# Performance work log

Hardware: AMD Instinct MI355X
Metric: run time of the kernel (lower is better)

## Reference

```python
import jax, jax.numpy as jnp
import numpy as np

NUM_HEAD = 8  # matches init_kwargs num_head


def setup_inputs() -> dict:
    key = jax.random.key(0)
    ks = jax.random.split(key, 8)
    B, N, C, P = 2, 1024, 512, 256
    cluster_num = 8
    s = 0.02
    return {
        "x_token": jax.random.normal(ks[0], (B, N, C), jnp.float32),
        "x_path": jax.random.normal(ks[1], (B, N, P), jnp.float32),
        "idx_cluster": jax.random.randint(ks[2], (B, N), 0, cluster_num),
        "cluster_num": cluster_num,
        "Wq": jax.random.normal(ks[3], (C, C), jnp.float32) * s,
        "Wk": jax.random.normal(ks[4], (C, C), jnp.float32) * s,
        "Wv": jax.random.normal(ks[5], (C, C), jnp.float32) * s,
        "Wproj": jax.random.normal(ks[6], (C, C), jnp.float32) * s,
        "bproj": jnp.zeros((C,), jnp.float32),
    }


def reference(x_token, x_path, idx_cluster, cluster_num, Wq, Wk, Wv, Wproj, bproj):
    eps = 1e-6
    B, N, C = x_token.shape
    H = NUM_HEAD
    hd = C // H
    scale = hd ** -0.5

    # Linear projections (torch Linear: y = x @ W^T), qkv_bias=False
    q = x_token @ Wq.T
    k = x_token @ Wk.T
    v = (x_token @ Wv.T).reshape(B, N, H, hd).transpose(0, 2, 1, 3)  # (B,H,N,hd)

    qh = q.reshape(B, N, H, hd).transpose(0, 2, 1, 3)  # (B,H,N,hd)
    kh = k.reshape(B, N, H, hd).transpose(0, 2, 1, 3)

    # Raw scaled scores, computed once instead of per-cluster scatter/repeat
    s_ = jnp.einsum('bhid,bhjd->bhij', qh, kh) * scale  # (B,H,N,N)

    # One-hot cluster membership: (B, cluster_num, N)
    m = (idx_cluster[:, None, :] == jnp.arange(cluster_num)[None, :, None]).astype(s_.dtype)

    # attn_map[b,c,h,i,j] = s_[b,h,i,j] if idx[b,i]==c and idx[b,j]==c else 0
    attn_map = s_[:, None] * m[:, :, None, :, None] * m[:, :, None, None, :]  # (B,K,H,N,N)

    # Sum over clusters -> within-cluster scores, zeros elsewhere
    attn = attn_map.sum(axis=1)  # (B,H,N,N)

    # Custom eps-smoothed exp normalization (masked_fill on exact zeros, as in source)
    attn = jnp.where(attn == 0, jnp.float32(-1e9), attn).astype(jnp.float32)
    attn = jnp.exp(attn)
    attn = (attn + eps / N) / (attn.sum(axis=-1, keepdims=True) + eps)

    out = jnp.einsum('bhij,bhjd->bhid', attn, v)  # (B,H,N,hd)
    out = out.transpose(0, 2, 1, 3).reshape(B, N, C)
    out = out @ Wproj.T + bproj
    return out, attn_map
```

## Files before the change

### kernel.cpp

```cpp
#include <hip/hip_runtime.h>
#include <hip/hip_bf16.h>
#include <cstdint>
#include <cstddef>

#define NB   2
#define NN   1024
#define NC   512
#define NH   8
#define NHD  64
#define NK   8

typedef __attribute__((ext_vector_type(8))) short short8v;
typedef __attribute__((ext_vector_type(4))) short short4v;
typedef __attribute__((ext_vector_type(4))) float f32x4;

__device__ __forceinline__ short f2bf(float f) {
    union { float f; unsigned u; } v; v.f = f;
    unsigned r = v.u + 0x7FFFu + ((v.u >> 16) & 1u);
    return (short)(r >> 16);
}
__device__ __forceinline__ float bf2f(short s) {
    union { unsigned u; float f; } v;
    v.u = ((unsigned)(unsigned short)s) << 16;
    return v.f;
}

__global__ __launch_bounds__(256) void cast_kernel(
    const float* __restrict__ x, const float* __restrict__ wq,
    const float* __restrict__ wk, const float* __restrict__ wv,
    const float* __restrict__ wp,
    short* __restrict__ xb, short* __restrict__ wqb, short* __restrict__ wkb,
    short* __restrict__ wvb, short* __restrict__ wpb) {
    int i = blockIdx.x * 256 + threadIdx.x;
    if (i < NB * NN * NC) xb[i] = f2bf(x[i]);
    if (i < NC * NC) {
        wqb[i] = f2bf(wq[i]);
        wkb[i] = f2bf(wk[i]);
        wvb[i] = f2bf(wv[i]);
        wpb[i] = f2bf(wp[i]);
    }
}

__global__ __launch_bounds__(256) void qkv_kernel(
    const short* __restrict__ xb, const short* __restrict__ wqb,
    const short* __restrict__ wkb, const short* __restrict__ wvb,
    short* __restrict__ qb, short* __restrict__ kb, short* __restrict__ vT) {
    __shared__ short As[64][40];
    __shared__ short Bs[64][40];
    const int tid = threadIdx.x;
    const int z = blockIdx.z;
    const short* Bsrc = (z == 0) ? wqb : ((z == 1) ? wkb : wvb);
    const int m0 = blockIdx.y * 64, n0 = blockIdx.x * 64;
    const int lane = tid & 63, wave = tid >> 6;
    const int wm = wave >> 1, wn = wave & 1, quad = lane >> 4, lr = lane & 15;
    const int row = tid >> 2, c0 = (tid & 3) * 8;
    f32x4 acc[2][2] = {};
    for (int kt = 0; kt < 512; kt += 32) {
        *(short8v*)&As[row][c0] = *(const short8v*)(xb + (m0 + row) * 512 + kt + c0);
        *(short8v*)&Bs[row][c0] = *(const short8v*)(Bsrc + (n0 + row) * 512 + kt + c0);
        __syncthreads();
        short8v a0 = *(short8v*)&As[wm * 32 + lr][quad * 8];
        short8v a1 = *(short8v*)&As[wm * 32 + 16 + lr][quad * 8];
        short8v b0 = *(short8v*)&Bs[wn * 32 + lr][quad * 8];
        short8v b1 = *(short8v*)&Bs[wn * 32 + 16 + lr][quad * 8];
        acc[0][0] = __builtin_amdgcn_mfma_f32_16x16x32_bf16(a0, b0, acc[0][0], 0, 0, 0);
        acc[0][1] = __builtin_amdgcn_mfma_f32_16x16x32_bf16(a0, b1, acc[0][1], 0, 0, 0);
        acc[1][0] = __builtin_amdgcn_mfma_f32_16x16x32_bf16(a1, b0, acc[1][0], 0, 0, 0);
        acc[1][1] = __builtin_amdgcn_mfma_f32_16x16x32_bf16(a1, b1, acc[1][1], 0, 0, 0);
        __syncthreads();
    }
    for (int sm = 0; sm < 2; sm++)
        for (int sn = 0; sn < 2; sn++)
            for (int r = 0; r < 4; r++) {
                int m = m0 + wm * 32 + sm * 16 + quad * 4 + r;
                int n = n0 + wn * 32 + sn * 16 + lr;
                short v = f2bf(acc[sm][sn][r]);
                if (z == 0) qb[m * 512 + n] = v;
                else if (z == 1) kb[m * 512 + n] = v;
                else {
                    int bb = m >> 10, i = m & 1023, h = n >> 6, d = n & 63;
                    vT[(size_t)(((bb * 8 + h) * 64 + d) << 10) + i] = v;
                }
            }
}

__global__ __launch_bounds__(256) void colsum_kernel(
    const short* __restrict__ vT, float* __restrict__ colsum) {
    __shared__ float cp[8][33];
    const int blk = blockIdx.x;
    const int bh = blk >> 3, dg = blk & 7;
    const int t = threadIdx.x;
    const int dl = t >> 5, seg = t & 31;
    const short* p = vT + (((size_t)(bh * 64 + dg * 8 + dl)) << 10) + seg * 32;
    float s = 0.f;
    for (int k = 0; k < 32; k += 8) {
        short8v v = *(const short8v*)(p + k);
        for (int j = 0; j < 8; j++) s += bf2f(v[j]);
    }
    cp[dl][seg] = s;
    __syncthreads();
    if (t < 8) {
        float v = 0.f;
        for (int s2 = 0; s2 < 32; s2++) v += cp[t][s2];
        colsum[bh * 64 + dg * 8 + t] = v;
    }
}

__global__ __launch_bounds__(256) void attn_fused_kernel(
    const short* __restrict__ qb, const short* __restrict__ kb,
    const short* __restrict__ vT, const int* __restrict__ idx,
    const float* __restrict__ colsum, float* __restrict__ attn,
    short* __restrict__ oh) {
    __shared__ short Qs[32][72], Ks[64][72], Vs[64][72], Es[32][72];
    __shared__ float Ss[32][68];
    __shared__ int idxi[32], idxj[64];
    __shared__ float rowpart[32][17];
    __shared__ float invL[32], csL[64];
    const int tid = threadIdx.x;
    const int z = blockIdx.y, b = z >> 3, h = z & 7;
    const int i0 = blockIdx.x * 32;
    const int lane = tid & 63, wave = tid >> 6;
    const int wm = wave >> 1, wn = wave & 1, quad = lane >> 4, lr = lane & 15;
    const int r0 = tid >> 3, cc = (tid & 7) * 8;
    *(short8v*)&Qs[r0][cc] = *(const short8v*)(qb + (b * 1024 + i0 + r0) * 512 + h * 64 + cc);
    if (tid < 32) idxi[tid] = idx[b * 1024 + i0 + tid];
    else if (tid < 96) csL[tid - 32] = colsum[z * 64 + (tid - 32)];
    f32x4 acc_o[2] = {};
    float rsum[2] = {0.f, 0.f};
    const int rL = tid >> 4, cI = tid & 15, cL = cI * 4;
    const f32x4 zero4 = {0.f, 0.f, 0.f, 0.f};
    for (int jt = 0; jt < 16; jt++) {
        const int j0 = jt * 64;
        *(short8v*)&Ks[r0][cc]      = *(const short8v*)(kb + (b * 1024 + j0 + r0) * 512 + h * 64 + cc);
        *(short8v*)&Ks[r0 + 32][cc] = *(const short8v*)(kb + (b * 1024 + j0 + r0 + 32) * 512 + h * 64 + cc);
        *(short8v*)&Vs[r0][cc]      = *(const short8v*)(vT + ((size_t)z << 16) + (r0 << 10) + j0 + cc);
        *(short8v*)&Vs[r0 + 32][cc] = *(const short8v*)(vT + ((size_t)z << 16) + ((r0 + 32) << 10) + j0 + cc);
        if (tid < 64) idxj[tid] = idx[b * 1024 + j0 + tid];
        __syncthreads();
        f32x4 as[2] = {};
        for (int k0 = 0; k0 < 64; k0 += 32) {
            short8v a0 = *(short8v*)&Qs[wm * 16 + lr][k0 + quad * 8];
            short8v b0 = *(short8v*)&Ks[wn * 32 + lr][k0 + quad * 8];
            short8v b1 = *(short8v*)&Ks[wn * 32 + 16 + lr][k0 + quad * 8];
            as[0] = __builtin_amdgcn_mfma_f32_16x16x32_bf16(a0, b0, as[0], 0, 0, 0);
            as[1] = __builtin_amdgcn_mfma_f32_16x16x32_bf16(a0, b1, as[1], 0, 0, 0);
        }
        for (int sn = 0; sn < 2; sn++)
            for (int r = 0; r < 4; r++)
                Ss[wm * 16 + quad * 4 + r][wn * 32 + sn * 16 + lr] = as[sn][r] * 0.125f;
        __syncthreads();
        for (int ii = 0; ii < 2; ii++) {
            const int row = ii * 16 + rL;
            const int ci = idxi[row];
            f32x4 s4 = *(f32x4*)&Ss[row][cL];
            f32x4 m4;
            short4v e4;
            for (int kk = 0; kk < 4; kk++) {
                const bool in = (idxj[cL + kk] == ci);
                const float sv = s4[kk];
                m4[kk] = in ? sv : 0.f;
                const float ev = (in && sv != 0.f) ? __expf(sv) : 0.f;
                rsum[ii] += ev;
                e4[kk] = f2bf(ev);
            }
            float* base = attn + (((size_t)(b * 64 + h)) << 20) + (((size_t)(i0 + row)) << 10) + j0 + cL;
            for (int c = 0; c < 8; c++) {
                f32x4 w = (c == ci) ? m4 : zero4;
                __builtin_nontemporal_store(w, (f32x4*)(base + ((size_t)c << 23)));
            }
            *(short4v*)&Es[row][cL] = e4;
        }
        __syncthreads();
        for (int k0 = 0; k0 < 64; k0 += 32) {
            short8v a0 = *(short8v*)&Es[wm * 16 + lr][k0 + quad * 8];
            short8v b0 = *(short8v*)&Vs[wn * 32 + lr][k0 + quad * 8];
            short8v b1 = *(short8v*)&Vs[wn * 32 + 16 + lr][k0 + quad * 8];
            acc_o[0] = __builtin_amdgcn_mfma_f32_16x16x32_bf16(a0, b0, acc_o[0], 0, 0, 0);
            acc_o[1] = __builtin_amdgcn_mfma_f32_16x16x32_bf16(a0, b1, acc_o[1], 0, 0, 0);
        }
        __syncthreads();
    }
    for (int ii = 0; ii < 2; ii++) rowpart[ii * 16 + rL][cI] = rsum[ii];
    __syncthreads();
    if (tid < 32) {
        float v = 0.f;
        for (int s = 0; s < 16; s++) v += rowpart[tid][s];
        invL[tid] = 1.f / (v + 1e-6f);
    }
    __syncthreads();
    const float epsN = 1e-6f / 1024.f;
    for (int sn = 0; sn < 2; sn++)
        for (int r = 0; r < 4; r++) {
            int iLoc = wm * 16 + quad * 4 + r;
            int d = wn * 32 + sn * 16 + lr;
            float val = (acc_o[sn][r] + epsN * csL[d]) * invL[iLoc];
            oh[((size_t)(b * 1024 + i0 + iLoc)) * 512 + h * 64 + d] = f2bf(val);
        }
}

__global__ __launch_bounds__(256) void proj_kernel(
    const short* __restrict__ oh, const short* __restrict__ wpb,
    const float* __restrict__ bias, float* __restrict__ out) {
    __shared__ short As[64][40];
    __shared__ short Bs[64][40];
    const int tid = threadIdx.x;
    const int m0 = blockIdx.y * 64, n0 = blockIdx.x * 64;
    const int lane = tid & 63, wave = tid >> 6;
    const int wm = wave >> 1, wn = wave & 1, quad = lane >> 4, lr = lane & 15;
    const int row = tid >> 2, c0 = (tid & 3) * 8;
    f32x4 acc[2][2] = {};
    for (int kt = 0; kt < 512; kt += 32) {
        *(short8v*)&As[row][c0] = *(const short8v*)(oh + (m0 + row) * 512 + kt + c0);
        *(short8v*)&Bs[row][c0] = *(const short8v*)(wpb + (n0 + row) * 512 + kt + c0);
        __syncthreads();
        short8v a0 = *(short8v*)&As[wm * 32 + lr][quad * 8];
        short8v a1 = *(short8v*)&As[wm * 32 + 16 + lr][quad * 8];
        short8v b0 = *(short8v*)&Bs[wn * 32 + lr][quad * 8];
        short8v b1 = *(short8v*)&Bs[wn * 32 + 16 + lr][quad * 8];
        acc[0][0] = __builtin_amdgcn_mfma_f32_16x16x32_bf16(a0, b0, acc[0][0], 0, 0, 0);
        acc[0][1] = __builtin_amdgcn_mfma_f32_16x16x32_bf16(a0, b1, acc[0][1], 0, 0, 0);
        acc[1][0] = __builtin_amdgcn_mfma_f32_16x16x32_bf16(a1, b0, acc[1][0], 0, 0, 0);
        acc[1][1] = __builtin_amdgcn_mfma_f32_16x16x32_bf16(a1, b1, acc[1][1], 0, 0, 0);
        __syncthreads();
    }
    for (int sm = 0; sm < 2; sm++)
        for (int sn = 0; sn < 2; sn++)
            for (int r = 0; r < 4; r++) {
                int m = m0 + wm * 32 + sm * 16 + quad * 4 + r;
                int n = n0 + wn * 32 + sn * 16 + lr;
                out[(size_t)m * 512 + n] = acc[sm][sn][r] + bias[n];
            }
}

extern "C" void kernel_launch(void* const* d_in, const int* in_sizes, int n_in,
                              void* d_out, int out_size, void* d_ws, size_t ws_size,
                              hipStream_t stream) {
    const float* x     = (const float*)d_in[0];
    const int*   idx   = (const int*)d_in[2];
    const float* Wq    = (const float*)d_in[4];
    const float* Wk    = (const float*)d_in[5];
    const float* Wv    = (const float*)d_in[6];
    const float* Wp    = (const float*)d_in[7];
    const float* bproj = (const float*)d_in[8];

    float* out  = (float*)d_out;
    float* attn = out + (size_t)NB * NN * NC;

    char* ws = (char*)d_ws;
    short* xb  = (short*)(ws + 0);
    short* wqb = (short*)(ws + 2097152);
    short* wkb = (short*)(ws + 2621440);
    short* wvb = (short*)(ws + 3145728);
    short* wpb = (short*)(ws + 3670016);
    short* qb  = (short*)(ws + 4194304);
    short* kb  = (short*)(ws + 6291456);
    short* vT  = (short*)(ws + 8388608);
    short* oh  = (short*)(ws + 10485760);
    float* colsum = (float*)(ws + 12582912);

    cast_kernel<<<4096, 256, 0, stream>>>(x, Wq, Wk, Wv, Wp, xb, wqb, wkb, wvb, wpb);
    qkv_kernel<<<dim3(8, 32, 3), 256, 0, stream>>>(xb, wqb, wkb, wvb, qb, kb, vT);
    colsum_kernel<<<128, 256, 0, stream>>>(vT, colsum);
    attn_fused_kernel<<<dim3(32, 16), 256, 0, stream>>>(qb, kb, vT, idx, colsum, attn, oh);
    proj_kernel<<<dim3(8, 32, 1), 256, 0, stream>>>(oh, wpb, bproj, out);
}
```

Before: 615.2 us.

## Fuse casts and colsum into GEMM/attention kernels, buffer attn_map rows in LDS

```diff
diff --git a/kernel.cpp b/kernel.cpp
--- a/kernel.cpp
+++ b/kernel.cpp
@@ -24,40 +24,32 @@
     v.u = ((unsigned)(unsigned short)s) << 16;
     return v.f;
 }
-
-__global__ __launch_bounds__(256) void cast_kernel(
+__device__ __forceinline__ short8v cvt8(const float* p) {
+    float4 a = *(const float4*)p;
+    float4 b = *(const float4*)(p + 4);
+    short8v r;
+    r[0] = f2bf(a.x); r[1] = f2bf(a.y); r[2] = f2bf(a.z); r[3] = f2bf(a.w);
+    r[4] = f2bf(b.x); r[5] = f2bf(b.y); r[6] = f2bf(b.z); r[7] = f2bf(b.w);
+    return r;
+}
+
+__global__ __launch_bounds__(256) void qkv_kernel(
     const float* __restrict__ x, const float* __restrict__ wq,
     const float* __restrict__ wk, const float* __restrict__ wv,
-    const float* __restrict__ wp,
-    short* __restrict__ xb, short* __restrict__ wqb, short* __restrict__ wkb,
-    short* __restrict__ wvb, short* __restrict__ wpb) {
-    int i = blockIdx.x * 256 + threadIdx.x;
-    if (i < NB * NN * NC) xb[i] = f2bf(x[i]);
-    if (i < NC * NC) {
-        wqb[i] = f2bf(wq[i]);
-        wkb[i] = f2bf(wk[i]);
-        wvb[i] = f2bf(wv[i]);
-        wpb[i] = f2bf(wp[i]);
-    }
-}
-
-__global__ __launch_bounds__(256) void qkv_kernel(
-    const short* __restrict__ xb, const short* __restrict__ wqb,
-    const short* __restrict__ wkb, const short* __restrict__ wvb,
     short* __restrict__ qb, short* __restrict__ kb, short* __restrict__ vT) {
     __shared__ short As[64][40];
     __shared__ short Bs[64][40];
     const int tid = threadIdx.x;
     const int z = blockIdx.z;
-    const short* Bsrc = (z == 0) ? wqb : ((z == 1) ? wkb : wvb);
+    const float* Bsrc = (z == 0) ? wq : ((z == 1) ? wk : wv);
     const int m0 = blockIdx.y * 64, n0 = blockIdx.x * 64;
     const int lane = tid & 63, wave = tid >> 6;
     const int wm = wave >> 1, wn = wave & 1, quad = lane >> 4, lr = lane & 15;
     const int row = tid >> 2, c0 = (tid & 3) * 8;
     f32x4 acc[2][2] = {};
     for (int kt = 0; kt < 512; kt += 32) {
-        *(short8v*)&As[row][c0] = *(const short8v*)(xb + (m0 + row) * 512 + kt + c0);
-        *(short8v*)&Bs[row][c0] = *(const short8v*)(Bsrc + (n0 + row) * 512 + kt + c0);
+        *(short8v*)&As[row][c0] = cvt8(x + (m0 + row) * 512 + kt + c0);
+        *(short8v*)&Bs[row][c0] = cvt8(Bsrc + (n0 + row) * 512 + kt + c0);
         __syncthreads();
         short8v a0 = *(short8v*)&As[wm * 32 + lr][quad * 8];
         short8v a1 = *(short8v*)&As[wm * 32 + 16 + lr][quad * 8];
@@ -84,122 +76,115 @@
             }
 }
 
-__global__ __launch_bounds__(256) void colsum_kernel(
-    const short* __restrict__ vT, float* __restrict__ colsum) {
-    __shared__ float cp[8][33];
-    const int blk = blockIdx.x;
-    const int bh = blk >> 3, dg = blk & 7;
-    const int t = threadIdx.x;
-    const int dl = t >> 5, seg = t & 31;
-    const short* p = vT + (((size_t)(bh * 64 + dg * 8 + dl)) << 10) + seg * 32;
-    float s = 0.f;
-    for (int k = 0; k < 32; k += 8) {
-        short8v v = *(const short8v*)(p + k);
-        for (int j = 0; j < 8; j++) s += bf2f(v[j]);
-    }
-    cp[dl][seg] = s;
-    __syncthreads();
-    if (t < 8) {
-        float v = 0.f;
-        for (int s2 = 0; s2 < 32; s2++) v += cp[t][s2];
-        colsum[bh * 64 + dg * 8 + t] = v;
-    }
-}
-
 __global__ __launch_bounds__(256) void attn_fused_kernel(
     const short* __restrict__ qb, const short* __restrict__ kb,
     const short* __restrict__ vT, const int* __restrict__ idx,
-    const float* __restrict__ colsum, float* __restrict__ attn,
-    short* __restrict__ oh) {
-    __shared__ short Qs[32][72], Ks[64][72], Vs[64][72], Es[32][72];
-    __shared__ float Ss[32][68];
-    __shared__ int idxi[32], idxj[64];
-    __shared__ float rowpart[32][17];
-    __shared__ float invL[32], csL[64];
+    float* __restrict__ attn, short* __restrict__ oh) {
+    __shared__ short Sm[16][1032];
+    __shared__ short Qs[16][72], Ks[64][72], Vs[64][72], Es[16][72];
+    __shared__ float Ss[16][68];
+    __shared__ float rowpart[16][17];
+    __shared__ float cpart[64][5];
+    __shared__ float invL[16], csL[64];
+    __shared__ int idxi[16], idxj[64];
     const int tid = threadIdx.x;
     const int z = blockIdx.y, b = z >> 3, h = z & 7;
-    const int i0 = blockIdx.x * 32;
+    const int i0 = blockIdx.x * 16;
     const int lane = tid & 63, wave = tid >> 6;
-    const int wm = wave >> 1, wn = wave & 1, quad = lane >> 4, lr = lane & 15;
-    const int r0 = tid >> 3, cc = (tid & 7) * 8;
-    *(short8v*)&Qs[r0][cc] = *(const short8v*)(qb + (b * 1024 + i0 + r0) * 512 + h * 64 + cc);
-    if (tid < 32) idxi[tid] = idx[b * 1024 + i0 + tid];
-    else if (tid < 96) csL[tid - 32] = colsum[z * 64 + (tid - 32)];
-    f32x4 acc_o[2] = {};
-    float rsum[2] = {0.f, 0.f};
+    const int quad = lane >> 4, lr = lane & 15;
+    const int r0 = tid >> 3, cc8 = (tid & 7) * 8;
     const int rL = tid >> 4, cI = tid & 15, cL = cI * 4;
-    const f32x4 zero4 = {0.f, 0.f, 0.f, 0.f};
+    {
+        int rq = tid >> 4, cq = (tid & 15) * 4;
+        *(short4v*)&Qs[rq][cq] = *(const short4v*)(qb + (b * 1024 + i0 + rq) * 512 + h * 64 + cq);
+    }
+    if (tid < 16) idxi[tid] = idx[b * 1024 + i0 + tid];
+    f32x4 acc_o = {};
+    float rsum = 0.f;
+    float csum = 0.f;
     for (int jt = 0; jt < 16; jt++) {
         const int j0 = jt * 64;
-        *(short8v*)&Ks[r0][cc]      = *(const short8v*)(kb + (b * 1024 + j0 + r0) * 512 + h * 64 + cc);
-        *(short8v*)&Ks[r0 + 32][cc] = *(const short8v*)(kb + (b * 1024 + j0 + r0 + 32) * 512 + h * 64 + cc);
-        *(short8v*)&Vs[r0][cc]      = *(const short8v*)(vT + ((size_t)z << 16) + (r0 << 10) + j0 + cc);
-        *(short8v*)&Vs[r0 + 32][cc] = *(const short8v*)(vT + ((size_t)z << 16) + ((r0 + 32) << 10) + j0 + cc);
+        *(short8v*)&Ks[r0][cc8]      = *(const short8v*)(kb + (b * 1024 + j0 + r0) * 512 + h * 64 + cc8);
+        *(short8v*)&Ks[r0 + 32][cc8] = *(const short8v*)(kb + (b * 1024 + j0 + r0 + 32) * 512 + h * 64 + cc8);
+        *(short8v*)&Vs[r0][cc8]      = *(const short8v*)(vT + ((size_t)z << 16) + (r0 << 10) + j0 + cc8);
+        *(short8v*)&Vs[r0 + 32][cc8] = *(const short8v*)(vT + ((size_t)z << 16) + ((r0 + 32) << 10) + j0 + cc8);
         if (tid < 64) idxj[tid] = idx[b * 1024 + j0 + tid];
         __syncthreads();
-        f32x4 as[2] = {};
+        {
+            const int d = tid >> 2, sg = (tid & 3) * 16;
+            for (int u = 0; u < 16; u++) csum += bf2f(Vs[d][sg + u]);
+        }
+        f32x4 as = {};
         for (int k0 = 0; k0 < 64; k0 += 32) {
-            short8v a0 = *(short8v*)&Qs[wm * 16 + lr][k0 + quad * 8];
-            short8v b0 = *(short8v*)&Ks[wn * 32 + lr][k0 + quad * 8];
-            short8v b1 = *(short8v*)&Ks[wn * 32 + 16 + lr][k0 + quad * 8];
-            as[0] = __builtin_amdgcn_mfma_f32_16x16x32_bf16(a0, b0, as[0], 0, 0, 0);
-            as[1] = __builtin_amdgcn_mfma_f32_16x16x32_bf16(a0, b1, as[1], 0, 0, 0);
-        }
-        for (int sn = 0; sn < 2; sn++)
-            for (int r = 0; r < 4; r++)
-                Ss[wm * 16 + quad * 4 + r][wn * 32 + sn * 16 + lr] = as[sn][r] * 0.125f;
-        __syncthreads();
-        for (int ii = 0; ii < 2; ii++) {
-            const int row = ii * 16 + rL;
-            const int ci = idxi[row];
-            f32x4 s4 = *(f32x4*)&Ss[row][cL];
-            f32x4 m4;
-            short4v e4;
+            short8v a0 = *(short8v*)&Qs[lr][k0 + quad * 8];
+            short8v b0 = *(short8v*)&Ks[wave * 16 + lr][k0 + quad * 8];
+            as = __builtin_amdgcn_mfma_f32_16x16x32_bf16(a0, b0, as, 0, 0, 0);
+        }
+        for (int r = 0; r < 4; r++)
+            Ss[quad * 4 + r][wave * 16 + lr] = as[r] * 0.125f;
+        __syncthreads();
+        {
+            const int ci = idxi[rL];
+            f32x4 s4 = *(f32x4*)&Ss[rL][cL];
+            short4v m4b, e4;
             for (int kk = 0; kk < 4; kk++) {
                 const bool in = (idxj[cL + kk] == ci);
                 const float sv = s4[kk];
-                m4[kk] = in ? sv : 0.f;
+                m4b[kk] = f2bf(in ? sv : 0.f);
                 const float ev = (in && sv != 0.f) ? __expf(sv) : 0.f;
-                rsum[ii] += ev;
+                rsum += ev;
                 e4[kk] = f2bf(ev);
             }
-            float* base = attn + (((size_t)(b * 64 + h)) << 20) + (((size_t)(i0 + row)) << 10) + j0 + cL;
-            for (int c = 0; c < 8; c++) {
-                f32x4 w = (c == ci) ? m4 : zero4;
-                __builtin_nontemporal_store(w, (f32x4*)(base + ((size_t)c << 23)));
-            }
-            *(short4v*)&Es[row][cL] = e4;
+            *(short4v*)&Sm[rL][j0 + cL] = m4b;
+            *(short4v*)&Es[rL][cL] = e4;
         }
         __syncthreads();
         for (int k0 = 0; k0 < 64; k0 += 32) {
-            short8v a0 = *(short8v*)&Es[wm * 16 + lr][k0 + quad * 8];
-            short8v b0 = *(short8v*)&Vs[wn * 32 + lr][k0 + quad * 8];
-            short8v b1 = *(short8v*)&Vs[wn * 32 + 16 + lr][k0 + quad * 8];
-            acc_o[0] = __builtin_amdgcn_mfma_f32_16x16x32_bf16(a0, b0, acc_o[0], 0, 0, 0);
-            acc_o[1] = __builtin_amdgcn_mfma_f32_16x16x32_bf16(a0, b1, acc_o[1], 0, 0, 0);
-        }
-        __syncthreads();
-    }
-    for (int ii = 0; ii < 2; ii++) rowpart[ii * 16 + rL][cI] = rsum[ii];
+            short8v a0 = *(short8v*)&Es[lr][k0 + quad * 8];
+            short8v b0 = *(short8v*)&Vs[wave * 16 + lr][k0 + quad * 8];
+            acc_o = __builtin_amdgcn_mfma_f32_16x16x32_bf16(a0, b0, acc_o, 0, 0, 0);
+        }
+        __syncthreads();
+    }
+    rowpart[rL][cI] = rsum;
+    cpart[tid >> 2][tid & 3] = csum;
     __syncthreads();
-    if (tid < 32) {
+    if (tid < 16) {
         float v = 0.f;
         for (int s = 0; s < 16; s++) v += rowpart[tid][s];
         invL[tid] = 1.f / (v + 1e-6f);
+    } else if (tid >= 64 && tid < 128) {
+        const int d = tid - 64;
+        csL[d] = cpart[d][0] + cpart[d][1] + cpart[d][2] + cpart[d][3];
     }
     __syncthreads();
-    const float epsN = 1e-6f / 1024.f;
-    for (int sn = 0; sn < 2; sn++)
+    {
+        const float epsN = 1e-6f / 1024.f;
         for (int r = 0; r < 4; r++) {
-            int iLoc = wm * 16 + quad * 4 + r;
-            int d = wn * 32 + sn * 16 + lr;
-            float val = (acc_o[sn][r] + epsN * csL[d]) * invL[iLoc];
+            int iLoc = quad * 4 + r;
+            int d = wave * 16 + lr;
+            float val = (acc_o[r] + epsN * csL[d]) * invL[iLoc];
             oh[((size_t)(b * 1024 + i0 + iLoc)) * 512 + h * 64 + d] = f2bf(val);
         }
+    }
+    const int tc = tid * 4;
+    const f32x4 zv = {0.f, 0.f, 0.f, 0.f};
+    for (int r = 0; r < 16; r++) {
+        const int ci = idxi[r];
+        short4v sm4 = *(short4v*)&Sm[r][tc];
+        f32x4 mv;
+        mv[0] = bf2f(sm4[0]); mv[1] = bf2f(sm4[1]);
+        mv[2] = bf2f(sm4[2]); mv[3] = bf2f(sm4[3]);
+        float* basebh = attn + (((size_t)(b * 64 + h)) << 20) + (((size_t)(i0 + r)) << 10) + tc;
+        for (int c = 0; c < 8; c++) {
+            f32x4 w = (c == ci) ? mv : zv;
+            *(f32x4*)(basebh + ((size_t)c << 23)) = w;
+        }
+    }
 }
 
 __global__ __launch_bounds__(256) void proj_kernel(
-    const short* __restrict__ oh, const short* __restrict__ wpb,
+    const short* __restrict__ oh, const float* __restrict__ wp,
     const float* __restrict__ bias, float* __restrict__ out) {
     __shared__ short As[64][40];
     __shared__ short Bs[64][40];
@@ -211,7 +196,7 @@
     f32x4 acc[2][2] = {};
     for (int kt = 0; kt < 512; kt += 32) {
         *(short8v*)&As[row][c0] = *(const short8v*)(oh + (m0 + row) * 512 + kt + c0);
-        *(short8v*)&Bs[row][c0] = *(const short8v*)(wpb + (n0 + row) * 512 + kt + c0);
+        *(short8v*)&Bs[row][c0] = cvt8(wp + (n0 + row) * 512 + kt + c0);
         __syncthreads();
         short8v a0 = *(short8v*)&As[wm * 32 + lr][quad * 8];
         short8v a1 = *(short8v*)&As[wm * 32 + 16 + lr][quad * 8];
@@ -247,20 +232,12 @@
     float* attn = out + (size_t)NB * NN * NC;
 
     char* ws = (char*)d_ws;
-    short* xb  = (short*)(ws + 0);
-    short* wqb = (short*)(ws + 2097152);
-    short* wkb = (short*)(ws + 2621440);
-    short* wvb = (short*)(ws + 3145728);
-    short* wpb = (short*)(ws + 3670016);
-    short* qb  = (short*)(ws + 4194304);
-    short* kb  = (short*)(ws + 6291456);
-    short* vT  = (short*)(ws + 8388608);
-    short* oh  = (short*)(ws + 10485760);
-    float* colsum = (float*)(ws + 12582912);
-
-    cast_kernel<<<4096, 256, 0, stream>>>(x, Wq, Wk, Wv, Wp, xb, wqb, wkb, wvb, wpb);
-    qkv_kernel<<<dim3(8, 32, 3), 256, 0, stream>>>(xb, wqb, wkb, wvb, qb, kb, vT);
-    colsum_kernel<<<128, 256, 0, stream>>>(vT, colsum);
-    attn_fused_kernel<<<dim3(32, 16), 256, 0, stream>>>(qb, kb, vT, idx, colsum, attn, oh);
-    proj_kernel<<<dim3(8, 32, 1), 256, 0, stream>>>(oh, wpb, bproj, out);
-}
+    short* qb = (short*)(ws + 0);
+    short* kb = (short*)(ws + 2097152);
+    short* vT = (short*)(ws + 4194304);
+    short* oh = (short*)(ws + 6291456);
+
+    qkv_kernel<<<dim3(8, 32, 3), 256, 0, stream>>>(x, Wq, Wk, Wv, qb, kb, vT);
+    attn_fused_kernel<<<dim3(64, 16), 256, 0, stream>>>(qb, kb, vT, idx, attn, oh);
+    proj_kernel<<<dim3(8, 32, 1), 256, 0, stream>>>(oh, Wp, bproj, out);
+}
```

Measured after the change: 618.7 us. About the same (+0.6%).
